# Kernel optimization log

Measured on AMD Instinct MI355X. Metric: run time of the kernel, lower is better.

The kernel has to match this reference:

```python
import jax, jax.numpy as jnp
import numpy as np

K = 7          # kernel_size
PAD = ((K - 1) * (1 - 1) + K) // 2  # = 3, 'same' padding for dilation=1


def setup_inputs() -> dict:
    key = jax.random.key(0)
    k1, k2 = jax.random.split(key)
    x = jax.random.normal(k1, (16, 96, 128, 128), dtype=jnp.float32)
    weight = jax.random.normal(k2, (96, K, K), dtype=jnp.float32) * 0.1
    return {"x": x, "weight": weight}


def reference(x, weight):
    """Morphological dilation2d with soft_max=True (ReLU after).

    Equivalent to torch: unfold(x, K, padding=PAD) -> max over window of
    (patch + w). nn.Unfold zero-pads, so borders see literal zeros in the max;
    we reproduce that with jnp.pad (zeros), not -inf padding.
    """
    B, C, H, W = x.shape
    xp = jnp.pad(x, ((0, 0), (0, 0), (PAD, PAD), (PAD, PAD)))  # zero pad, matches nn.Unfold
    out = jnp.full((B, C, H, W), -jnp.inf, dtype=x.dtype)
    # Fixed K*K loop over kernel taps (structural, not data-dim loop):
    # running max avoids materializing the (B,H*W,C,K*K) im2col tensor.
    for i in range(K):
        for j in range(K):
            shifted = jax.lax.dynamic_slice(xp, (0, 0, i, j), (B, C, H, W))
            out = jnp.maximum(out, shifted + weight[None, :, i, j, None, None])
    return jax.nn.relu(out)  # soft_max=True -> ReLU activation
```

## Files before the change

kernel.cpp:

```cpp
#include <hip/hip_runtime.h>

#define HH 128
#define WW 128
#define CC 96
#define KK 7


__device__ __forceinline__ void load_row(float* d, const float* __restrict__ xp,
                                         int r, int tc0, bool lok, bool rok) {
  if ((unsigned)r < (unsigned)HH) {
    const float* p = xp + r * WW + tc0 - 4;
    float4 a, b, c;
    if (lok) a = *(const float4*)(p);
    else     a = make_float4(0.f, 0.f, 0.f, 0.f);
    b = *(const float4*)(p + 4);
    if (rok) c = *(const float4*)(p + 8);
    else     c = make_float4(0.f, 0.f, 0.f, 0.f);
    d[0] = a.x; d[1] = a.y; d[2] = a.z; d[3] = a.w;
    d[4] = b.x; d[5] = b.y; d[6] = b.z; d[7] = b.w;
    d[8] = c.x; d[9] = c.y; d[10] = c.z; d[11] = c.w;
  } else {
#pragma unroll
    for (int i = 0; i < 12; ++i) d[i] = 0.f;
  }
}

__global__ __launch_bounds__(256) void morph_kernel(
    const float* __restrict__ x, const float* __restrict__ weight,
    float* __restrict__ out) {
  const int t = threadIdx.x;
  const int cg = t & 31;
  const int rg = t >> 5;
  const int half = blockIdx.x & 1;
  const int plane = blockIdx.x >> 1;
  const int c = plane % CC;

  const float* __restrict__ xp = x + (size_t)plane * (HH * WW);
  float* __restrict__ op = out + (size_t)plane * (HH * WW);
  const float* __restrict__ Wc = weight + c * (KK * KK);

  float wv[KK * KK];
#pragma unroll
  for (int k = 0; k < KK * KK; ++k)
    wv[k] = __int_as_float(__builtin_amdgcn_readfirstlane(__float_as_int(Wc[k])));

  const int tc0 = cg << 2;
  const int row0 = half * 64 + rg * 8;
  const bool lok = (tc0 >= 4);
  const bool rok = (tc0 <= WW - 8);

  float acc[8][4];
#pragma unroll
  for (int y = 0; y < 8; ++y)
#pragma unroll
    for (int q = 0; q < 4; ++q) acc[y][q] = 0.f;

#pragma unroll
  for (int s = 0; s < 14; ++s) {
    float d[12];
    load_row(d, xp, row0 - 3 + s, tc0, lok, rok);

#pragma unroll
    for (int yl = 0; yl < 8; ++yl) {
      const int i = s - yl;
      if (i < 0 || i >= KK) continue;
      const float w0 = wv[i * 7 + 0], w1 = wv[i * 7 + 1], w2 = wv[i * 7 + 2],
                  w3 = wv[i * 7 + 3], w4 = wv[i * 7 + 4], w5 = wv[i * 7 + 5],
                  w6 = wv[i * 7 + 6];
#pragma unroll
      for (int q = 0; q < 4; ++q) {
        const float t0 = d[q + 1] + w0;
        const float t1 = d[q + 2] + w1;
        const float t2 = d[q + 3] + w2;
        const float t3 = d[q + 4] + w3;
        const float t4 = d[q + 5] + w4;
        const float t5 = d[q + 6] + w5;
        const float t6 = d[q + 7] + w6;
        float m = acc[yl][q];
        m = fmaxf(fmaxf(m, t0), t1);
        m = fmaxf(fmaxf(m, t2), t3);
        m = fmaxf(fmaxf(m, t4), t5);
        m = fmaxf(m, t6);
        acc[yl][q] = m;
      }
    }

    if (s >= 6) {
      const int yl = s - 6;
      float4 o = make_float4(acc[yl][0], acc[yl][1], acc[yl][2], acc[yl][3]);
      *(float4*)(op + (size_t)(row0 + yl) * WW + tc0) = o;
    }
  }
}

extern "C" void kernel_launch(void* const* d_in, const int* in_sizes, int n_in,
                              void* d_out, int out_size, void* d_ws, size_t ws_size,
                              hipStream_t stream) {
  const float* x = (const float*)d_in[0];
  const float* w = (const float*)d_in[1];
  float* out = (float*)d_out;
  const int nblocks = 16 * CC * 2;
  morph_kernel<<<nblocks, 256, 0, stream>>>(x, w, out);
}
```

Baseline: 192.3 us.

## Stage padded input tile in LDS before computing dilation rows

Each block cooperatively loads its 70-row zero-padded input slab into shared memory, then threads read their 12-wide row windows from LDS instead of global memory. This removes redundant overlapping global loads and the boundary branches. In exchange it uses about 38KB of LDS per block, adds a barrier, and serialises the load phase before compute, which may reduce occupancy.

```diff
diff --git a/kernel.cpp b/kernel.cpp
--- a/kernel.cpp
+++ b/kernel.cpp
@@ -6,31 +6,16 @@
 #define KK 7
 
 
-__device__ __forceinline__ void load_row(float* d, const float* __restrict__ xp,
-                                         int r, int tc0, bool lok, bool rok) {
-  if ((unsigned)r < (unsigned)HH) {
-    const float* p = xp + r * WW + tc0 - 4;
-    float4 a, b, c;
-    if (lok) a = *(const float4*)(p);
-    else     a = make_float4(0.f, 0.f, 0.f, 0.f);
-    b = *(const float4*)(p + 4);
-    if (rok) c = *(const float4*)(p + 8);
-    else     c = make_float4(0.f, 0.f, 0.f, 0.f);
-    d[0] = a.x; d[1] = a.y; d[2] = a.z; d[3] = a.w;
-    d[4] = b.x; d[5] = b.y; d[6] = b.z; d[7] = b.w;
-    d[8] = c.x; d[9] = c.y; d[10] = c.z; d[11] = c.w;
-  } else {
-#pragma unroll
-    for (int i = 0; i < 12; ++i) d[i] = 0.f;
-  }
-}
+#define LROWS 70
+#define LW 136
+#define LSLOTS (LROWS * (LW / 4))
 
 __global__ __launch_bounds__(256) void morph_kernel(
     const float* __restrict__ x, const float* __restrict__ weight,
     float* __restrict__ out) {
+  __shared__ float lds[LROWS * LW];
+
   const int t = threadIdx.x;
-  const int cg = t & 31;
-  const int rg = t >> 5;
   const int half = blockIdx.x & 1;
   const int plane = blockIdx.x >> 1;
   const int c = plane % CC;
@@ -44,10 +29,28 @@
   for (int k = 0; k < KK * KK; ++k)
     wv[k] = __int_as_float(__builtin_amdgcn_readfirstlane(__float_as_int(Wc[k])));
 
+  const int r0g = half * 64 - 3;
+#pragma unroll
+  for (int k = 0; k < (LSLOTS + 255) / 256; ++k) {
+    const unsigned idx = k * 256 + t;
+    if (idx < LSLOTS) {
+      const unsigned row = idx / 34;
+      const unsigned c4 = idx - row * 34;
+      const int gr = r0g + (int)row;
+      float4 v = make_float4(0.f, 0.f, 0.f, 0.f);
+      if ((unsigned)gr < (unsigned)HH && c4 >= 1 && c4 <= 32) {
+        v = *(const float4*)(xp + gr * WW + (c4 - 1) * 4);
+      }
+      *(float4*)(&lds[row * LW + c4 * 4]) = v;
+    }
+  }
+  __syncthreads();
+
+  const int cg = t & 31;
+  const int rg = t >> 5;
   const int tc0 = cg << 2;
   const int row0 = half * 64 + rg * 8;
-  const bool lok = (tc0 >= 4);
-  const bool rok = (tc0 <= WW - 8);
+  const float* __restrict__ lp = &lds[(rg * 8) * LW + tc0];
 
   float acc[8][4];
 #pragma unroll
@@ -58,7 +61,14 @@
 #pragma unroll
   for (int s = 0; s < 14; ++s) {
     float d[12];
-    load_row(d, xp, row0 - 3 + s, tc0, lok, rok);
+    {
+      const float4 A = *(const float4*)(lp + s * LW);
+      const float4 B = *(const float4*)(lp + s * LW + 4);
+      const float4 C = *(const float4*)(lp + s * LW + 8);
+      d[0] = A.x; d[1] = A.y; d[2] = A.z; d[3] = A.w;
+      d[4] = B.x; d[5] = B.y; d[6] = B.z; d[7] = B.w;
+      d[8] = C.x; d[9] = C.y; d[10] = C.z; d[11] = C.w;
+    }
 
 #pragma unroll
     for (int yl = 0; yl < 8; ++yl) {
```

New measurement: 200.6 us. 4.3% more time.

## Process whole plane per block with two column strips and double-buffered row loads

Applied to the files above, without the earlier changes.

Each block now covers a full 128x128 plane, and each thread computes two 4-wide column strips 64 apart instead of one. Input rows are prefetched one step ahead into a double-buffered register set, which hides global load latency. Border handling changes from branching on the loads to clamped pointers plus value selects. Register pressure roughly doubles, and the launch bounds hint of 3 blocks may cause spills or lower occupancy.

```diff
diff --git a/kernel.cpp b/kernel.cpp
--- a/kernel.cpp
+++ b/kernel.cpp
@@ -6,33 +6,13 @@
 #define KK 7
 
 
-__device__ __forceinline__ void load_row(float* d, const float* __restrict__ xp,
-                                         int r, int tc0, bool lok, bool rok) {
-  if ((unsigned)r < (unsigned)HH) {
-    const float* p = xp + r * WW + tc0 - 4;
-    float4 a, b, c;
-    if (lok) a = *(const float4*)(p);
-    else     a = make_float4(0.f, 0.f, 0.f, 0.f);
-    b = *(const float4*)(p + 4);
-    if (rok) c = *(const float4*)(p + 8);
-    else     c = make_float4(0.f, 0.f, 0.f, 0.f);
-    d[0] = a.x; d[1] = a.y; d[2] = a.z; d[3] = a.w;
-    d[4] = b.x; d[5] = b.y; d[6] = b.z; d[7] = b.w;
-    d[8] = c.x; d[9] = c.y; d[10] = c.z; d[11] = c.w;
-  } else {
-#pragma unroll
-    for (int i = 0; i < 12; ++i) d[i] = 0.f;
-  }
-}
-
-__global__ __launch_bounds__(256) void morph_kernel(
+__global__ __launch_bounds__(256, 3) void morph_kernel(
     const float* __restrict__ x, const float* __restrict__ weight,
     float* __restrict__ out) {
   const int t = threadIdx.x;
-  const int cg = t & 31;
-  const int rg = t >> 5;
-  const int half = blockIdx.x & 1;
-  const int plane = blockIdx.x >> 1;
+  const int cg = t & 15;
+  const int rg = t >> 4;
+  const int plane = blockIdx.x;
   const int c = plane % CC;
 
   const float* __restrict__ xp = x + (size_t)plane * (HH * WW);
@@ -45,20 +25,57 @@
     wv[k] = __int_as_float(__builtin_amdgcn_readfirstlane(__float_as_int(Wc[k])));
 
   const int tc0 = cg << 2;
-  const int row0 = half * 64 + rg * 8;
+  const int row0 = rg << 3;
   const bool lok = (tc0 >= 4);
-  const bool rok = (tc0 <= WW - 8);
+  const bool rok2 = (tc0 + 64 <= WW - 8);
 
-  float acc[8][4];
+  const float* pb = xp + (row0 - 3) * WW + (tc0 - 4);
+  const float* q0 = lok ? pb : pb + 4;
+  const float* q1 = pb + 4;
+  const float* q2 = pb + 8;
+  const float* q3 = pb + 64;
+  const float* q4 = pb + 68;
+  const float* q5 = rok2 ? pb + 72 : pb + 68;
+
+  float4 S1[2][3], S2[2][3];
+
+#define LOAD_STRIP(slot, s)                                                  \
+  do {                                                                       \
+    const int r_ = row0 - 3 + (s);                                           \
+    if ((unsigned)r_ < (unsigned)HH) {                                       \
+      S1[slot][0] = *(const float4*)(q0 + (s) * WW);                         \
+      S1[slot][1] = *(const float4*)(q1 + (s) * WW);                         \
+      S1[slot][2] = *(const float4*)(q2 + (s) * WW);                         \
+      S2[slot][0] = *(const float4*)(q3 + (s) * WW);                         \
+      S2[slot][1] = *(const float4*)(q4 + (s) * WW);                         \
+      S2[slot][2] = *(const float4*)(q5 + (s) * WW);                         \
+    } else {                                                                 \
+      const float4 z_ = make_float4(0.f, 0.f, 0.f, 0.f);                     \
+      S1[slot][0] = z_; S1[slot][1] = z_; S1[slot][2] = z_;                  \
+      S2[slot][0] = z_; S2[slot][1] = z_; S2[slot][2] = z_;                  \
+    }                                                                        \
+  } while (0)
+
+  float acc1[8][4], acc2[8][4];
 #pragma unroll
   for (int y = 0; y < 8; ++y)
 #pragma unroll
-    for (int q = 0; q < 4; ++q) acc[y][q] = 0.f;
+    for (int q = 0; q < 4; ++q) { acc1[y][q] = 0.f; acc2[y][q] = 0.f; }
+
+  LOAD_STRIP(0, 0);
 
 #pragma unroll
   for (int s = 0; s < 14; ++s) {
-    float d[12];
-    load_row(d, xp, row0 - 3 + s, tc0, lok, rok);
+    if (s + 1 < 14) LOAD_STRIP((s + 1) & 1, s + 1);
+
+    const int sl = s & 1;
+    const float4 A1 = S1[sl][0], B1 = S1[sl][1], C1 = S1[sl][2];
+    const float4 A2 = S2[sl][0], B2 = S2[sl][1], C2 = S2[sl][2];
+    const float e1[10] = {lok ? A1.y : 0.f, lok ? A1.z : 0.f, lok ? A1.w : 0.f,
+                          B1.x, B1.y, B1.z, B1.w, C1.x, C1.y, C1.z};
+    const float e2[10] = {A2.y, A2.z, A2.w, B2.x, B2.y, B2.z, B2.w,
+                          rok2 ? C2.x : 0.f, rok2 ? C2.y : 0.f,
+                          rok2 ? C2.z : 0.f};
 
 #pragma unroll
     for (int yl = 0; yl < 8; ++yl) {
@@ -69,28 +86,47 @@
                   w6 = wv[i * 7 + 6];
 #pragma unroll
       for (int q = 0; q < 4; ++q) {
-        const float t0 = d[q + 1] + w0;
-        const float t1 = d[q + 2] + w1;
-        const float t2 = d[q + 3] + w2;
-        const float t3 = d[q + 4] + w3;
-        const float t4 = d[q + 5] + w4;
-        const float t5 = d[q + 6] + w5;
-        const float t6 = d[q + 7] + w6;
-        float m = acc[yl][q];
-        m = fmaxf(fmaxf(m, t0), t1);
-        m = fmaxf(fmaxf(m, t2), t3);
-        m = fmaxf(fmaxf(m, t4), t5);
-        m = fmaxf(m, t6);
-        acc[yl][q] = m;
+        {
+          const float t0 = e1[q + 0] + w0;
+          const float t1 = e1[q + 1] + w1;
+          const float t2 = e1[q + 2] + w2;
+          const float t3 = e1[q + 3] + w3;
+          const float t4 = e1[q + 4] + w4;
+          const float t5 = e1[q + 5] + w5;
+          const float t6 = e1[q + 6] + w6;
+          float m = acc1[yl][q];
+          m = fmaxf(fmaxf(m, t0), t1);
+          m = fmaxf(fmaxf(m, t2), t3);
+          m = fmaxf(fmaxf(m, t4), t5);
+          acc1[yl][q] = fmaxf(m, t6);
+        }
+        {
+          const float t0 = e2[q + 0] + w0;
+          const float t1 = e2[q + 1] + w1;
+          const float t2 = e2[q + 2] + w2;
+          const float t3 = e2[q + 3] + w3;
+          const float t4 = e2[q + 4] + w4;
+          const float t5 = e2[q + 5] + w5;
+          const float t6 = e2[q + 6] + w6;
+          float m = acc2[yl][q];
+          m = fmaxf(fmaxf(m, t0), t1);
+          m = fmaxf(fmaxf(m, t2), t3);
+          m = fmaxf(fmaxf(m, t4), t5);
+          acc2[yl][q] = fmaxf(m, t6);
+        }
       }
     }
 
     if (s >= 6) {
       const int yl = s - 6;
-      float4 o = make_float4(acc[yl][0], acc[yl][1], acc[yl][2], acc[yl][3]);
-      *(float4*)(op + (size_t)(row0 + yl) * WW + tc0) = o;
+      float* orow = op + (size_t)(row0 + yl) * WW + tc0;
+      *(float4*)(orow) =
+          make_float4(acc1[yl][0], acc1[yl][1], acc1[yl][2], acc1[yl][3]);
+      *(float4*)(orow + 64) =
+          make_float4(acc2[yl][0], acc2[yl][1], acc2[yl][2], acc2[yl][3]);
     }
   }
+#undef LOAD_STRIP
 }
 
 extern "C" void kernel_launch(void* const* d_in, const int* in_sizes, int n_in,
@@ -99,6 +135,6 @@
   const float* x = (const float*)d_in[0];
   const float* w = (const float*)d_in[1];
   float* out = (float*)d_out;
-  const int nblocks = 16 * CC * 2;
+  const int nblocks = 16 * CC;
   morph_kernel<<<nblocks, 256, 0, stream>>>(x, w, out);
 }
```

Result: slower. 244.2 us (+27.0%).

## Stage input half-plane in LDS via direct global-to-LDS loads

Applied to the files above, without the earlier changes.

Each block now copies its 70-row halo region (67 rows of input plus a zero border row) into shared memory using global_load_lds, then reads row strips from LDS with double-buffered register prefetch. This replaces repeated overlapping global loads per thread, which fetched each row many times across row groups, with a single cooperative load. The cost is a 35KB LDS footprint per block, which limits occupancy (launch bounds now ask for 4 blocks), plus a full barrier before compute with no overlap of load and compute.

```diff
diff --git a/kernel.cpp b/kernel.cpp
--- a/kernel.cpp
+++ b/kernel.cpp
@@ -5,32 +5,25 @@
 #define CC 96
 #define KK 7
 
+#define LROWS 70
+#define LF (LROWS * WW)
+#define NSLOT ((67 * WW) / 4)
 
-__device__ __forceinline__ void load_row(float* d, const float* __restrict__ xp,
-                                         int r, int tc0, bool lok, bool rok) {
-  if ((unsigned)r < (unsigned)HH) {
-    const float* p = xp + r * WW + tc0 - 4;
-    float4 a, b, c;
-    if (lok) a = *(const float4*)(p);
-    else     a = make_float4(0.f, 0.f, 0.f, 0.f);
-    b = *(const float4*)(p + 4);
-    if (rok) c = *(const float4*)(p + 8);
-    else     c = make_float4(0.f, 0.f, 0.f, 0.f);
-    d[0] = a.x; d[1] = a.y; d[2] = a.z; d[3] = a.w;
-    d[4] = b.x; d[5] = b.y; d[6] = b.z; d[7] = b.w;
-    d[8] = c.x; d[9] = c.y; d[10] = c.z; d[11] = c.w;
-  } else {
-#pragma unroll
-    for (int i = 0; i < 12; ++i) d[i] = 0.f;
-  }
+
+typedef __attribute__((address_space(1))) const void gv_t;
+typedef __attribute__((address_space(3))) void lv_t;
+
+__device__ __forceinline__ void gload_lds16(const float* g, float* l) {
+  __builtin_amdgcn_global_load_lds((gv_t*)g, (lv_t*)(unsigned)(uintptr_t)l,
+                                   16, 0, 0);
 }
 
-__global__ __launch_bounds__(256) void morph_kernel(
+__global__ __launch_bounds__(256, 4) void morph_kernel(
     const float* __restrict__ x, const float* __restrict__ weight,
     float* __restrict__ out) {
+  __shared__ float lds[LF];
+
   const int t = threadIdx.x;
-  const int cg = t & 31;
-  const int rg = t >> 5;
   const int half = blockIdx.x & 1;
   const int plane = blockIdx.x >> 1;
   const int c = plane % CC;
@@ -44,10 +37,36 @@
   for (int k = 0; k < KK * KK; ++k)
     wv[k] = __int_as_float(__builtin_amdgcn_readfirstlane(__float_as_int(Wc[k])));
 
+  const int rv0 = half ? 0 : 3;
+  const int zrow0 = half ? 67 : 0;
+  const int grow0 = half ? 61 : 0;
+
+  if (t < 96) {
+    *(float4*)&lds[zrow0 * WW + t * 4] = make_float4(0.f, 0.f, 0.f, 0.f);
+  }
+
+  {
+    const float* gsrc = xp + grow0 * WW;
+    float* ldst = &lds[rv0 * WW];
+#pragma unroll
+    for (int k = 0; k < 9; ++k) {
+      const int slot = k * 256 + t;
+      if (slot < NSLOT) gload_lds16(gsrc + slot * 4, ldst + slot * 4);
+    }
+  }
+  __syncthreads();
+
+  const int cg = t & 31;
+  const int rg = t >> 5;
   const int tc0 = cg << 2;
-  const int row0 = half * 64 + rg * 8;
+  const int r0l = rg << 3;
   const bool lok = (tc0 >= 4);
   const bool rok = (tc0 <= WW - 8);
+
+  const float* lp = &lds[r0l * WW + tc0];
+  const float* qA = lok ? lp - 4 : lp;
+  const float* qB = lp;
+  const float* qC = rok ? lp + 4 : lp;
 
   float acc[8][4];
 #pragma unroll
@@ -55,10 +74,25 @@
 #pragma unroll
     for (int q = 0; q < 4; ++q) acc[y][q] = 0.f;
 
+  float4 S[2][3];
+#define LOAD_STRIP(slot, s)                      \
+  do {                                           \
+    S[slot][0] = *(const float4*)(qA + (s) * WW); \
+    S[slot][1] = *(const float4*)(qB + (s) * WW); \
+    S[slot][2] = *(const float4*)(qC + (s) * WW); \
+  } while (0)
+
+  LOAD_STRIP(0, 0);
+
 #pragma unroll
   for (int s = 0; s < 14; ++s) {
-    float d[12];
-    load_row(d, xp, row0 - 3 + s, tc0, lok, rok);
+    if (s + 1 < 14) LOAD_STRIP((s + 1) & 1, s + 1);
+
+    const int sl = s & 1;
+    const float4 A = S[sl][0], B = S[sl][1], C = S[sl][2];
+    const float e[10] = {lok ? A.y : 0.f, lok ? A.z : 0.f, lok ? A.w : 0.f,
+                         B.x, B.y, B.z, B.w,
+                         rok ? C.x : 0.f, rok ? C.y : 0.f, rok ? C.z : 0.f};
 
 #pragma unroll
     for (int yl = 0; yl < 8; ++yl) {
@@ -69,28 +103,28 @@
                   w6 = wv[i * 7 + 6];
 #pragma unroll
       for (int q = 0; q < 4; ++q) {
-        const float t0 = d[q + 1] + w0;
-        const float t1 = d[q + 2] + w1;
-        const float t2 = d[q + 3] + w2;
-        const float t3 = d[q + 4] + w3;
-        const float t4 = d[q + 5] + w4;
-        const float t5 = d[q + 6] + w5;
-        const float t6 = d[q + 7] + w6;
+        const float t0 = e[q + 0] + w0;
+        const float t1 = e[q + 1] + w1;
+        const float t2 = e[q + 2] + w2;
+        const float t3 = e[q + 3] + w3;
+        const float t4 = e[q + 4] + w4;
+        const float t5 = e[q + 5] + w5;
+        const float t6 = e[q + 6] + w6;
         float m = acc[yl][q];
         m = fmaxf(fmaxf(m, t0), t1);
         m = fmaxf(fmaxf(m, t2), t3);
         m = fmaxf(fmaxf(m, t4), t5);
-        m = fmaxf(m, t6);
-        acc[yl][q] = m;
+        acc[yl][q] = fmaxf(m, t6);
       }
     }
 
     if (s >= 6) {
       const int yl = s - 6;
       float4 o = make_float4(acc[yl][0], acc[yl][1], acc[yl][2], acc[yl][3]);
-      *(float4*)(op + (size_t)(row0 + yl) * WW + tc0) = o;
+      *(float4*)(op + (size_t)(half * 64 + r0l + yl) * WW + tc0) = o;
     }
   }
+#undef LOAD_STRIP
 }
 
 extern "C" void kernel_launch(void* const* d_in, const int* in_sizes, int n_in,
```

After: 184.6 us. 4.0% less time.
